# Kernel tuning notes

Hardware: AMD Instinct MI355X
Metric: run time of the kernel (lower is better)

The kernel has to match this reference:

```python
import jax, jax.numpy as jnp
import numpy as np

N, D, H = 512, 512, 1024  # n tokens, per-token dim, hidden; input_dim = 2*D


def setup_inputs() -> dict:
    key = jax.random.key(0)
    k1, k2, k3, k4, k5 = jax.random.split(key, 5)
    inp = jax.random.normal(k1, (N, D), dtype=jnp.float32)
    # torch nn.Linear stores weight [out, in]; we store transposed [in, out]
    s1 = 1.0 / np.sqrt(2 * D)
    W1 = jax.random.uniform(k2, (2 * D, H), dtype=jnp.float32, minval=-s1, maxval=s1)
    b1 = jax.random.uniform(k3, (H,), dtype=jnp.float32, minval=-s1, maxval=s1)
    s2 = 1.0 / np.sqrt(H)
    W2 = jax.random.uniform(k4, (H, 1), dtype=jnp.float32, minval=-s2, maxval=s2)
    b2 = jax.random.uniform(k5, (1,), dtype=jnp.float32, minval=-s2, maxval=s2)
    return {"input": inp, "W1": W1, "b1": b1, "W2": W2, "b2": b2}


def reference(input, W1, b1, W2, b2):
    x = jnp.squeeze(input)                       # [n, d]
    d = x.shape[1]
    # cat(x[i], x[j]) @ W1 == x[i] @ W1[:d] + x[j] @ W1[d:]
    hi = x @ W1[:d]                              # [n, h]
    hj = x @ W1[d:]                              # [n, h]
    h = jnp.tanh(hi[:, None, :] + hj[None, :, :] + b1)  # [n, n, h]
    scores = h @ W2 + b2                         # [n, n, 1]
    return scores[..., 0]                        # [n, n]
```

## Files before the change

### kernel.cpp

```cpp
#include <hip/hip_runtime.h>
#include <math.h>

#define NN 512
#define DD 512
#define HH 1024
#define C2LOG2E 2.8853900817779268f

typedef __attribute__((ext_vector_type(8))) short bf16x8;
typedef __attribute__((ext_vector_type(4))) float f32x4;

static __device__ __forceinline__ float rcp_fast(float x) {
    return __builtin_amdgcn_rcpf(x);
}
static __device__ __forceinline__ float exp2_fast(float x) {
    return __builtin_amdgcn_exp2f(x);
}
static __device__ __forceinline__ ushort f2bf(float f) {
    unsigned u = __float_as_uint(f);
    u += 0x7FFF + ((u >> 16) & 1);
    return (ushort)(u >> 16);
}

__global__ __launch_bounds__(256) void k_convert(const float* __restrict__ x,
                                                 const float* __restrict__ W1,
                                                 const float* __restrict__ b2,
                                                 short* __restrict__ xb,
                                                 short* __restrict__ Bt,
                                                 float* __restrict__ out) {
    __shared__ float ts[64][65];
    const int t = threadIdx.x;
    const int bx = blockIdx.x;
    if (bx < 256) {
        const int f4 = bx * 256 + t;
        const float4 v = *(const float4*)&x[f4 * 4];
        ushort4 o;
        o.x = f2bf(v.x); o.y = f2bf(v.y); o.z = f2bf(v.z); o.w = f2bf(v.w);
        *(ushort4*)&xb[f4 * 4] = o;
        return;
    }
    if (bx >= 512) {
        const int f4 = (bx - 512) * 256 + t;
        const float b = b2[0];
        float4 o; o.x = b; o.y = b; o.z = b; o.w = b;
        ((float4*)out)[f4] = o;
        return;
    }
    const int tid = bx - 256;
    const int k0 = (tid >> 5) * 64;
    const int nglob = (tid & 31) * 64;
    const int off = (nglob >= 1024) ? 512 : 0;
    const int nm = nglob & 1023;
#pragma unroll
    for (int u = 0; u < 4; ++u) {
        const int f4 = t + u * 256;
        const int r = f4 >> 4, c = (f4 & 15) * 4;
        *(float4*)&ts[r][c] = *(const float4*)&W1[(off + k0 + r) * HH + nm + c];
    }
    __syncthreads();
#pragma unroll
    for (int u = 0; u < 4; ++u) {
        const int idx = t + u * 256;
        const int nn = idx >> 4, k4 = (idx & 15) * 4;
        ushort4 o;
        o.x = f2bf(ts[k4 + 0][nn]);
        o.y = f2bf(ts[k4 + 1][nn]);
        o.z = f2bf(ts[k4 + 2][nn]);
        o.w = f2bf(ts[k4 + 3][nn]);
        *(ushort4*)&Bt[(nglob + nn) * DD + k0 + k4] = o;
    }
}

__global__ __launch_bounds__(256) void k_gemm_mfma(const short* __restrict__ xb,
                                                   const short* __restrict__ Bt,
                                                   const float* __restrict__ b1,
                                                   float* __restrict__ E) {
    const int t = threadIdx.x;
    const int w = t >> 6, l = t & 63;
    const int i0 = blockIdx.x * 64 + w * 16;
    const int n0 = blockIdx.y * 32;
    const int lm = l & 15;
    const int krow = (l >> 4) * 8;

    f32x4 acc[2] = {};
    const short* xp  = xb + (i0 + lm) * DD + krow;
    const short* bp0 = Bt + (n0 + 0 * 16 + lm) * DD + krow;
    const short* bp1 = Bt + (n0 + 1 * 16 + lm) * DD + krow;
#pragma unroll
    for (int kt = 0; kt < DD; kt += 32) {
        const bf16x8 a = *(const bf16x8*)(xp + kt);
        acc[0] = __builtin_amdgcn_mfma_f32_16x16x32_bf16(a, *(const bf16x8*)(bp0 + kt), acc[0], 0, 0, 0);
        acc[1] = __builtin_amdgcn_mfma_f32_16x16x32_bf16(a, *(const bf16x8*)(bp1 + kt), acc[1], 0, 0, 0);
    }
    const int orow = i0 + (l >> 4) * 4;
#pragma unroll
    for (int c = 0; c < 2; ++c) {
        const int n = n0 + c * 16 + lm;
        const float badd = (n >= HH) ? b1[n - HH] : 0.0f;
#pragma unroll
        for (int r = 0; r < 4; ++r) {
            E[(orow + r) * (2 * HH) + n] = exp2_fast(C2LOG2E * (acc[c][r] + badd));
        }
    }
}

__global__ __launch_bounds__(256) void k_score(const float* __restrict__ E,
                                               const float* __restrict__ W2,
                                               float* __restrict__ out) {
    __shared__ float e1s[64][68];
    __shared__ float e2s[64][68];
    __shared__ float w2s[64];
    const int t = threadIdx.x;
    const int i0 = blockIdx.x * 64, j0 = blockIdx.y * 64;
    const int z = blockIdx.z;
    const int hb = z * 64;
    const int tx = t & 15, ty = t >> 4;

#pragma unroll
    for (int u = 0; u < 4; ++u) {
        const int f4 = t + u * 256;
        const int r = f4 >> 4, c = (f4 & 15) * 4;
        *(float4*)&e1s[r][c] = *(const float4*)&E[(i0 + r) * (2 * HH) + hb + c];
        *(float4*)&e2s[r][c] = *(const float4*)&E[(j0 + r) * (2 * HH) + HH + hb + c];
    }
    if (t < 64) w2s[t] = W2[hb + t];
    __syncthreads();

    float acc[4][4] = {};
    float sw = 0.0f;
    const float* e1p = &e1s[ty * 4][0];
    const float* e2p = &e2s[tx][0];
#pragma unroll 4
    for (int hq = 0; hq < 16; ++hq) {
        const int h = hq * 4;
        const float4 w = *(const float4*)&w2s[h];
        float4 ev[4], fv[4];
#pragma unroll
        for (int m = 0; m < 4; ++m) ev[m] = *(const float4*)(e1p + m * 68 + h);
#pragma unroll
        for (int n = 0; n < 4; ++n) fv[n] = *(const float4*)(e2p + n * 16 * 68 + h);
#pragma unroll
        for (int m = 0; m < 4; ++m) {
#pragma unroll
            for (int n = 0; n < 4; ++n) {
                const float d0 = __builtin_fmaf(ev[m].x, fv[n].x, 1.0f);
                const float d1 = __builtin_fmaf(ev[m].y, fv[n].y, 1.0f);
                const float d2 = __builtin_fmaf(ev[m].z, fv[n].z, 1.0f);
                const float d3 = __builtin_fmaf(ev[m].w, fv[n].w, 1.0f);
                const float d01 = d0 * d1;
                const float d23 = d2 * d3;
                const float n01 = __builtin_fmaf(w.x, d1, w.y * d0);
                const float n23 = __builtin_fmaf(w.z, d3, w.w * d2);
                const float Nn  = __builtin_fmaf(n01, d23, n23 * d01);
                const float Dd  = d01 * d23;
                acc[m][n] = __builtin_fmaf(Nn, rcp_fast(Dd), acc[m][n]);
            }
        }
        sw += w.x + w.y + w.z + w.w;
    }

#pragma unroll
    for (int m = 0; m < 4; ++m) {
        const int row = i0 + ty * 4 + m;
#pragma unroll
        for (int n = 0; n < 4; ++n) {
            const int col = j0 + tx + n * 16;
            atomicAdd(&out[row * NN + col], sw - 2.0f * acc[m][n]);
        }
    }
}

extern "C" void kernel_launch(void* const* d_in, const int* in_sizes, int n_in,
                              void* d_out, int out_size, void* d_ws, size_t ws_size,
                              hipStream_t stream) {
    const float* x  = (const float*)d_in[0];
    const float* W1 = (const float*)d_in[1];
    const float* b1 = (const float*)d_in[2];
    const float* W2 = (const float*)d_in[3];
    const float* b2 = (const float*)d_in[4];
    float* out = (float*)d_out;

    float* E  = (float*)d_ws;
    short* xb = (short*)(E + NN * 2 * HH);
    short* Bt = xb + NN * DD;

    k_convert<<<dim3(768), 256, 0, stream>>>(x, W1, b2, xb, Bt, out);
    k_gemm_mfma<<<dim3(8, 64), 256, 0, stream>>>(xb, Bt, b1, E);
    k_score<<<dim3(8, 8, 16), 256, 0, stream>>>(E, W2, out);
}
```

Measured before the change: 50.41 us.

## Store intermediate E in bf16 and pre-swizzle GEMM operands into MFMA fragment order

The exp-transformed activations E are now written as bf16 instead of fp32, which halves the global traffic between the GEMM and score kernels and halves the score kernel's shared-memory footprint. The convert kernel writes x and W1 directly in MFMA fragment order so each lane's GEMM loads are contiguous. The score inner loop now processes 8 hidden units per step, computing two reciprocals per group of four. The bf16 rounding of E adds error to the tanh-based scores, and the extra bf16-to-float unpacking adds ALU work in the score kernel.

```diff
diff --git a/kernel.cpp b/kernel.cpp
--- a/kernel.cpp
+++ b/kernel.cpp
@@ -20,32 +20,42 @@
     u += 0x7FFF + ((u >> 16) & 1);
     return (ushort)(u >> 16);
 }
+static __device__ __forceinline__ float bf2f(short u) {
+    return __uint_as_float(((unsigned)(ushort)u) << 16);
+}
 
 __global__ __launch_bounds__(256) void k_convert(const float* __restrict__ x,
                                                  const float* __restrict__ W1,
                                                  const float* __restrict__ b2,
-                                                 short* __restrict__ xb,
-                                                 short* __restrict__ Bt,
+                                                 short* __restrict__ xbs,
+                                                 short* __restrict__ Bts,
                                                  float* __restrict__ out) {
     __shared__ float ts[64][65];
     const int t = threadIdx.x;
     const int bx = blockIdx.x;
-    if (bx < 256) {
-        const int f4 = bx * 256 + t;
-        const float4 v = *(const float4*)&x[f4 * 4];
-        ushort4 o;
-        o.x = f2bf(v.x); o.y = f2bf(v.y); o.z = f2bf(v.z); o.w = f2bf(v.w);
-        *(ushort4*)&xb[f4 * 4] = o;
+    if (bx < 128) {
+        const int q = bx * 256 + t;
+        const int g = q >> 10, ktc = (q >> 6) & 15, l = q & 63;
+        const int i = g * 16 + (l & 15);
+        const int k0 = ktc * 32 + (l >> 4) * 8;
+        const float4 v0 = *(const float4*)&x[i * DD + k0];
+        const float4 v1 = *(const float4*)&x[i * DD + k0 + 4];
+        bf16x8 o;
+        o[0] = (short)f2bf(v0.x); o[1] = (short)f2bf(v0.y);
+        o[2] = (short)f2bf(v0.z); o[3] = (short)f2bf(v0.w);
+        o[4] = (short)f2bf(v1.x); o[5] = (short)f2bf(v1.y);
+        o[6] = (short)f2bf(v1.z); o[7] = (short)f2bf(v1.w);
+        *(bf16x8*)&xbs[q * 8] = o;
         return;
     }
-    if (bx >= 512) {
-        const int f4 = (bx - 512) * 256 + t;
+    if (bx >= 384) {
+        const int f4 = (bx - 384) * 256 + t;
         const float b = b2[0];
         float4 o; o.x = b; o.y = b; o.z = b; o.w = b;
         ((float4*)out)[f4] = o;
         return;
     }
-    const int tid = bx - 256;
+    const int tid = bx - 128;
     const int k0 = (tid >> 5) * 64;
     const int nglob = (tid & 31) * 64;
     const int off = (nglob >= 1024) ? 512 : 0;
@@ -58,109 +68,131 @@
     }
     __syncthreads();
 #pragma unroll
-    for (int u = 0; u < 4; ++u) {
-        const int idx = t + u * 256;
-        const int nn = idx >> 4, k4 = (idx & 15) * 4;
-        ushort4 o;
-        o.x = f2bf(ts[k4 + 0][nn]);
-        o.y = f2bf(ts[k4 + 1][nn]);
-        o.z = f2bf(ts[k4 + 2][nn]);
-        o.w = f2bf(ts[k4 + 3][nn]);
-        *(ushort4*)&Bt[(nglob + nn) * DD + k0 + k4] = o;
-    }
-}
-
-__global__ __launch_bounds__(256) void k_gemm_mfma(const short* __restrict__ xb,
-                                                   const short* __restrict__ Bt,
+    for (int u = 0; u < 2; ++u) {
+        const int q = u * 256 + t;
+        const int lg = q >> 7, lc = (q >> 6) & 1, l = q & 63;
+        const int n_loc = lg * 16 + (l & 15);
+        const int k_loc = lc * 32 + (l >> 4) * 8;
+        bf16x8 o;
+#pragma unroll
+        for (int j = 0; j < 8; ++j) o[j] = (short)f2bf(ts[k_loc + j][n_loc]);
+        const int gg = (nglob >> 4) + lg;
+        const int ktc = (k0 >> 5) + lc;
+        *(bf16x8*)&Bts[((gg * 16 + ktc) * 64 + l) * 8] = o;
+    }
+}
+
+__global__ __launch_bounds__(256) void k_gemm_mfma(const short* __restrict__ xbs,
+                                                   const short* __restrict__ Bts,
                                                    const float* __restrict__ b1,
-                                                   float* __restrict__ E) {
+                                                   short* __restrict__ Ebf) {
     const int t = threadIdx.x;
     const int w = t >> 6, l = t & 63;
-    const int i0 = blockIdx.x * 64 + w * 16;
-    const int n0 = blockIdx.y * 32;
+    const int gi = blockIdx.x * 4 + w;
+    const int by = blockIdx.y;
+    const int gn0 = by * 2;
+
+    f32x4 acc[2] = {};
+    const short* ap  = xbs + gi * 8192 + l * 8;
+    const short* bp0 = Bts + (gn0 + 0) * 8192 + l * 8;
+    const short* bp1 = Bts + (gn0 + 1) * 8192 + l * 8;
+#pragma unroll
+    for (int ktc = 0; ktc < 16; ++ktc) {
+        const bf16x8 a = *(const bf16x8*)(ap + ktc * 512);
+        acc[0] = __builtin_amdgcn_mfma_f32_16x16x32_bf16(a, *(const bf16x8*)(bp0 + ktc * 512), acc[0], 0, 0, 0);
+        acc[1] = __builtin_amdgcn_mfma_f32_16x16x32_bf16(a, *(const bf16x8*)(bp1 + ktc * 512), acc[1], 0, 0, 0);
+    }
     const int lm = l & 15;
-    const int krow = (l >> 4) * 8;
-
-    f32x4 acc[2] = {};
-    const short* xp  = xb + (i0 + lm) * DD + krow;
-    const short* bp0 = Bt + (n0 + 0 * 16 + lm) * DD + krow;
-    const short* bp1 = Bt + (n0 + 1 * 16 + lm) * DD + krow;
-#pragma unroll
-    for (int kt = 0; kt < DD; kt += 32) {
-        const bf16x8 a = *(const bf16x8*)(xp + kt);
-        acc[0] = __builtin_amdgcn_mfma_f32_16x16x32_bf16(a, *(const bf16x8*)(bp0 + kt), acc[0], 0, 0, 0);
-        acc[1] = __builtin_amdgcn_mfma_f32_16x16x32_bf16(a, *(const bf16x8*)(bp1 + kt), acc[1], 0, 0, 0);
-    }
-    const int orow = i0 + (l >> 4) * 4;
+    const int orow = gi * 16 + (l >> 4) * 4;
+    const bool second = (by >= 32);
 #pragma unroll
     for (int c = 0; c < 2; ++c) {
-        const int n = n0 + c * 16 + lm;
-        const float badd = (n >= HH) ? b1[n - HH] : 0.0f;
+        const int n = by * 32 + c * 16 + lm;
+        const float badd = second ? b1[n - HH] : 0.0f;
 #pragma unroll
         for (int r = 0; r < 4; ++r) {
-            E[(orow + r) * (2 * HH) + n] = exp2_fast(C2LOG2E * (acc[c][r] + badd));
-        }
-    }
-}
-
-__global__ __launch_bounds__(256) void k_score(const float* __restrict__ E,
+            Ebf[(orow + r) * (2 * HH) + n] =
+                (short)f2bf(exp2_fast(C2LOG2E * (acc[c][r] + badd)));
+        }
+    }
+}
+
+__global__ __launch_bounds__(256) void k_score(const short* __restrict__ Ebf,
                                                const float* __restrict__ W2,
                                                float* __restrict__ out) {
-    __shared__ float e1s[64][68];
-    __shared__ float e2s[64][68];
+    __shared__ short e1s[64][72];
+    __shared__ short e2s[64][72];
     __shared__ float w2s[64];
     const int t = threadIdx.x;
     const int i0 = blockIdx.x * 64, j0 = blockIdx.y * 64;
-    const int z = blockIdx.z;
-    const int hb = z * 64;
+    const int hb = blockIdx.z * 64;
     const int tx = t & 15, ty = t >> 4;
 
 #pragma unroll
-    for (int u = 0; u < 4; ++u) {
-        const int f4 = t + u * 256;
-        const int r = f4 >> 4, c = (f4 & 15) * 4;
-        *(float4*)&e1s[r][c] = *(const float4*)&E[(i0 + r) * (2 * HH) + hb + c];
-        *(float4*)&e2s[r][c] = *(const float4*)&E[(j0 + r) * (2 * HH) + HH + hb + c];
+    for (int u = 0; u < 2; ++u) {
+        const int q = u * 256 + t;
+        const int r = q >> 3, c8 = (q & 7) * 8;
+        *(bf16x8*)&e1s[r][c8] = *(const bf16x8*)&Ebf[(i0 + r) * (2 * HH) + hb + c8];
+        *(bf16x8*)&e2s[r][c8] = *(const bf16x8*)&Ebf[(j0 + r) * (2 * HH) + HH + hb + c8];
     }
     if (t < 64) w2s[t] = W2[hb + t];
     __syncthreads();
 
     float acc[4][4] = {};
     float sw = 0.0f;
-    const float* e1p = &e1s[ty * 4][0];
-    const float* e2p = &e2s[tx][0];
-#pragma unroll 4
-    for (int hq = 0; hq < 16; ++hq) {
-        const int h = hq * 4;
-        const float4 w = *(const float4*)&w2s[h];
-        float4 ev[4], fv[4];
-#pragma unroll
-        for (int m = 0; m < 4; ++m) ev[m] = *(const float4*)(e1p + m * 68 + h);
-#pragma unroll
-        for (int n = 0; n < 4; ++n) fv[n] = *(const float4*)(e2p + n * 16 * 68 + h);
+    const int ty4 = ty * 4;
+#pragma unroll 2
+    for (int hq = 0; hq < 64; hq += 8) {
+        float ef[4][8], ff[4][8];
 #pragma unroll
         for (int m = 0; m < 4; ++m) {
+            const bf16x8 v = *(const bf16x8*)&e1s[ty4 + m][hq];
+#pragma unroll
+            for (int j = 0; j < 8; ++j) ef[m][j] = bf2f(v[j]);
+        }
+#pragma unroll
+        for (int n = 0; n < 4; ++n) {
+            const bf16x8 v = *(const bf16x8*)&e2s[tx + n * 16][hq];
+#pragma unroll
+            for (int j = 0; j < 8; ++j) ff[n][j] = bf2f(v[j]);
+        }
+        const float4 wl = *(const float4*)&w2s[hq];
+        const float4 wh = *(const float4*)&w2s[hq + 4];
+#pragma unroll
+        for (int m = 0; m < 4; ++m) {
 #pragma unroll
             for (int n = 0; n < 4; ++n) {
-                const float d0 = __builtin_fmaf(ev[m].x, fv[n].x, 1.0f);
-                const float d1 = __builtin_fmaf(ev[m].y, fv[n].y, 1.0f);
-                const float d2 = __builtin_fmaf(ev[m].z, fv[n].z, 1.0f);
-                const float d3 = __builtin_fmaf(ev[m].w, fv[n].w, 1.0f);
-                const float d01 = d0 * d1;
-                const float d23 = d2 * d3;
-                const float n01 = __builtin_fmaf(w.x, d1, w.y * d0);
-                const float n23 = __builtin_fmaf(w.z, d3, w.w * d2);
-                const float Nn  = __builtin_fmaf(n01, d23, n23 * d01);
-                const float Dd  = d01 * d23;
-                acc[m][n] = __builtin_fmaf(Nn, rcp_fast(Dd), acc[m][n]);
+                const float* em = ef[m];
+                const float* fn = ff[n];
+                const float d0 = __builtin_fmaf(em[0], fn[0], 1.0f);
+                const float d1 = __builtin_fmaf(em[1], fn[1], 1.0f);
+                const float d2 = __builtin_fmaf(em[2], fn[2], 1.0f);
+                const float d3 = __builtin_fmaf(em[3], fn[3], 1.0f);
+                const float d4 = __builtin_fmaf(em[4], fn[4], 1.0f);
+                const float d5 = __builtin_fmaf(em[5], fn[5], 1.0f);
+                const float d6 = __builtin_fmaf(em[6], fn[6], 1.0f);
+                const float d7 = __builtin_fmaf(em[7], fn[7], 1.0f);
+                const float d01 = d0 * d1, d23 = d2 * d3;
+                const float d45 = d4 * d5, d67 = d6 * d7;
+                const float n01 = __builtin_fmaf(wl.x, d1, wl.y * d0);
+                const float n23 = __builtin_fmaf(wl.z, d3, wl.w * d2);
+                const float n45 = __builtin_fmaf(wh.x, d5, wh.y * d4);
+                const float n67 = __builtin_fmaf(wh.z, d7, wh.w * d6);
+                const float N1 = __builtin_fmaf(n01, d23, n23 * d01);
+                const float N2 = __builtin_fmaf(n45, d67, n67 * d45);
+                const float D1 = d01 * d23, D2 = d45 * d67;
+                float a = acc[m][n];
+                a = __builtin_fmaf(N1, rcp_fast(D1), a);
+                a = __builtin_fmaf(N2, rcp_fast(D2), a);
+                acc[m][n] = a;
             }
         }
-        sw += w.x + w.y + w.z + w.w;
+        sw += wl.x + wl.y + wl.z + wl.w + wh.x + wh.y + wh.z + wh.w;
     }
 
 #pragma unroll
     for (int m = 0; m < 4; ++m) {
-        const int row = i0 + ty * 4 + m;
+        const int row = i0 + ty4 + m;
 #pragma unroll
         for (int n = 0; n < 4; ++n) {
             const int col = j0 + tx + n * 16;
@@ -179,11 +211,11 @@
     const float* b2 = (const float*)d_in[4];
     float* out = (float*)d_out;
 
-    float* E  = (float*)d_ws;
-    short* xb = (short*)(E + NN * 2 * HH);
-    short* Bt = xb + NN * DD;
-
-    k_convert<<<dim3(768), 256, 0, stream>>>(x, W1, b2, xb, Bt, out);
-    k_gemm_mfma<<<dim3(8, 64), 256, 0, stream>>>(xb, Bt, b1, E);
-    k_score<<<dim3(8, 8, 16), 256, 0, stream>>>(E, W2, out);
-}
+    short* Ebf = (short*)d_ws;
+    short* xbs = Ebf + NN * 2 * HH;
+    short* Bts = xbs + NN * DD;
+
+    k_convert<<<dim3(640), 256, 0, stream>>>(x, W1, b2, xbs, Bts, out);
+    k_gemm_mfma<<<dim3(8, 64), 256, 0, stream>>>(xbs, Bts, b1, Ebf);
+    k_score<<<dim3(8, 8, 16), 256, 0, stream>>>(Ebf, W2, out);
+}
```

Measured after the change: 43.13 us. -14.4%, faster.
